# Performance work log

Measured on AMD Instinct MI355X. Metric: run time of the kernel, lower is better.

## Reference

```python
import jax, jax.numpy as jnp
import numpy as np

CHANNELS = 10
LENGTH = 64
DEPTH = 4
BATCH = 2048


def setup_inputs() -> dict:
    key = jax.random.key(0)
    x = jax.random.normal(key, (BATCH, CHANNELS * LENGTH), dtype=jnp.float32)
    return {"x": x}


def _seg_exp(dx, depth):
    # Signature of a single linear segment with increment dx: (B, C).
    # Level k is dx^{(x)k} / k! (flattened to (B, C^k)).
    b = dx.shape[0]
    terms = [dx]
    for k in range(2, depth + 1):
        t = jnp.einsum('bi,bj->bij', terms[-1], dx).reshape(b, -1) / k
        terms.append(t)
    return tuple(terms)


def _chen(a, b, depth):
    # Truncated tensor-algebra product (Chen's identity), both with scalar part 1.
    # (A (x) B)_k = A_k + B_k + sum_{i=1}^{k-1} A_i (x) B_{k-i}
    bsz = a[0].shape[0]
    out = []
    for k in range(1, depth + 1):
        t = a[k - 1] + b[k - 1]
        for i in range(1, k):
            t = t + jnp.einsum('bi,bj->bij', a[i - 1], b[k - i - 1]).reshape(bsz, -1)
        out.append(t)
    return tuple(out)


def signature(path, depth):
    # path: (B, C, L). Increments along the path (last) dimension.
    dx = (path[:, :, 1:] - path[:, :, :-1]).transpose(0, 2, 1)  # (B, L-1, C)
    init = _seg_exp(dx[:, 0], depth)

    def step(carry, dxt):
        return _chen(carry, _seg_exp(dxt, depth), depth), None

    sig, _ = jax.lax.scan(step, init, dx[:, 1:].transpose(1, 0, 2))  # scan over L-2 steps
    return jnp.concatenate(sig, axis=-1)  # (B, sum_k C^k)


def reference(x):
    path = x.reshape(x.shape[0], CHANNELS, LENGTH)
    return signature(path, DEPTH)
```

## Files before the change

### kernel.cpp

```cpp
#include <hip/hip_runtime.h>
#include <hip/hip_bf16.h>


typedef short short8 __attribute__((ext_vector_type(8)));
typedef float f2 __attribute__((ext_vector_type(2)));
typedef float f4 __attribute__((ext_vector_type(4)));
typedef float f32x4 __attribute__((ext_vector_type(4)));
typedef unsigned int uint4v __attribute__((ext_vector_type(4)));

constexpr int C = 10, L = 64, T = 63;
constexpr int OUTSZ = 10 + 100 + 1000 + 10000;
constexpr int SP = 68;
constexpr int KS = 64;

__device__ __forceinline__ unsigned packbf(float lo, float hi) {
  union { __hip_bfloat162 h; unsigned u; } cv;
  cv.h = __float22bfloat162_rn(make_float2(lo, hi));
  return cv.u;
}
__device__ __forceinline__ int swz(int row, int k) {
  return row * KS + ((((k >> 3) ^ (row & 7)) << 3) | (k & 7));
}

__global__ __launch_bounds__(512, 6) void sig4_kernel(
    const float* __restrict__ x, float* __restrict__ out)
{
  __shared__ __align__(16) unsigned char smem_raw[45120];
  unsigned short* Ab = (unsigned short*)smem_raw;
  unsigned short* Ub = (unsigned short*)(smem_raw + 12800);
  unsigned short* Bb = (unsigned short*)(smem_raw + 25600);
  float* dxT = (float*)(smem_raw + 39680);
  float* PsT = (float*)(smem_raw + 42400);

  const int t = threadIdx.x;
  const int w = t >> 6, lane = t & 63;
  const float* __restrict__ xb = x + (size_t)blockIdx.x * (C * L);
  float* __restrict__ ob = out + (size_t)blockIdx.x * OUTSZ;

  for (int i = t; i < C * SP; i += 512) {
    int c = i / SP, s = i - c * SP;
    float v = 0.f;
    if (s < T) v = xb[c * L + s + 1] - xb[c * L + s];
    dxT[i] = v;
  }
  __syncthreads();
  for (int c = w; c < C; c += 8) {
    float v = (lane > 0) ? dxT[c * SP + lane - 1] : 0.f;
    #pragma unroll
    for (int d = 1; d < 64; d <<= 1) {
      float y = __shfl_up(v, d);
      if (lane >= d) v += y;
    }
    PsT[c * SP + lane] = v;
  }
  if (t < 40) PsT[(t >> 2) * SP + 64 + (t & 3)] = 0.f;
  __syncthreads();

  if (t < 100) {
    const int i_ = t / 10, j_ = t - (t / 10) * 10;
    const float* dip = dxT + i_ * SP;
    const float* pp  = PsT + i_ * SP;
    const float* djp = dxT + j_ * SP;
    float s2 = 0.f;
    #pragma unroll
    for (int ch = 0; ch < 8; ++ch) {
      f4 d0 = *(const f4*)(dip + ch * 8), d1 = *(const f4*)(dip + ch * 8 + 4);
      f4 p0 = *(const f4*)(pp  + ch * 8), p1 = *(const f4*)(pp  + ch * 8 + 4);
      f4 e0 = *(const f4*)(djp + ch * 8), e1 = *(const f4*)(djp + ch * 8 + 4);
      float di[8] = {d0.x, d0.y, d0.z, d0.w, d1.x, d1.y, d1.z, d1.w};
      float pv[8] = {p0.x, p0.y, p0.z, p0.w, p1.x, p1.y, p1.z, p1.w};
      float dj[8] = {e0.x, e0.y, e0.z, e0.w, e1.x, e1.y, e1.z, e1.w};
      float bu[8], bv[8], zz[8];
      #pragma unroll
      for (int e = 0; e < 8; ++e) {
        bu[e] = fmaf(di[e], 0.25f, pv[e]) * (dj[e] * (1.f / 3.f));
        bv[e] = fmaf(di[e], (1.f / 3.f), pv[e]) * (dj[e] * 0.5f);
        zz[e] = fmaf(di[e], 0.5f, pv[e]) * dj[e];
      }
      float u2v[8], v2v[8];
      #pragma unroll
      for (int e = 0; e < 8; ++e) {
        u2v[e] = bu[e] + s2;
        v2v[e] = bv[e] + s2;
        s2 += zz[e];
      }
      uint4v vp, up;
      #pragma unroll
      for (int q = 0; q < 4; ++q) {
        vp[q] = packbf(v2v[2 * q], v2v[2 * q + 1]);
        up[q] = packbf(u2v[2 * q], u2v[2 * q + 1]);
      }
      *(uint4v*)&Ab[swz(t, ch * 8)] = vp;
      *(uint4v*)&Ub[swz(t, ch * 8)] = up;
    }
    ob[10 + t] = s2;
    if (j_ == 0) ob[i_] = PsT[i_ * SP + 63];
  } else if (t >= 128) {
    const int q = t - 128;
    for (int task = q; task < 110 * 8; task += 384) {
      const int col = task >> 3, ch = task & 7;
      const int base = ch * 8;
      float b1v[8];
      if (col < 100) {
        const int k2 = col / 10, l2 = col - (col / 10) * 10;
        const float* dk = dxT + k2 * SP;
        const float* pl = PsT + l2 * SP;
        const float S1l = pl[63];
        f4 d0 = *(const f4*)(dk + base), d1 = *(const f4*)(dk + base + 4);
        f4 pa = *(const f4*)(pl + base), pb = *(const f4*)(pl + base + 4);
        f4 pc = *(const f4*)(pl + base + 8);
        float dv[8] = {d0.x, d0.y, d0.z, d0.w, d1.x, d1.y, d1.z, d1.w};
        float Pn[8] = {pa.y, pa.z, pa.w, pb.x, pb.y, pb.z, pb.w, pc.x};
        #pragma unroll
        for (int e = 0; e < 8; ++e) b1v[e] = dv[e] * (S1l - Pn[e]);
      } else {
        const float* dk = dxT + (col - 100) * SP;
        f4 d0 = *(const f4*)(dk + base), d1 = *(const f4*)(dk + base + 4);
        b1v[0] = d0.x; b1v[1] = d0.y; b1v[2] = d0.z; b1v[3] = d0.w;
        b1v[4] = d1.x; b1v[5] = d1.y; b1v[6] = d1.z; b1v[7] = d1.w;
      }
      uint4v pk;
      #pragma unroll
      for (int qq = 0; qq < 4; ++qq) pk[qq] = packbf(b1v[2 * qq], b1v[2 * qq + 1]);
      *(uint4v*)&Bb[swz(col, base)] = pk;
    }
  }
  __syncthreads();

  const int lm = lane & 15, lg = lane >> 4;
  f32x4 acc[7];
  #pragma unroll
  for (int ct = 0; ct < 7; ++ct) acc[ct] = f32x4{0.f, 0.f, 0.f, 0.f};

  if (w < 7) {
    const int arow = w * 16 + lm;
    short8 a0 = (arow < 100) ? *(const short8*)&Ab[swz(arow, lg * 8)]
                             : short8{0, 0, 0, 0, 0, 0, 0, 0};
    short8 a1 = (arow < 100) ? *(const short8*)&Ab[swz(arow, 32 + lg * 8)]
                             : short8{0, 0, 0, 0, 0, 0, 0, 0};
    #pragma unroll
    for (int ct = 0; ct < 7; ++ct) {
      const int bcol = ct * 16 + lm;
      short8 b0 = (bcol < 110) ? *(const short8*)&Bb[swz(bcol, lg * 8)]
                               : short8{0, 0, 0, 0, 0, 0, 0, 0};
      short8 b1 = (bcol < 110) ? *(const short8*)&Bb[swz(bcol, 32 + lg * 8)]
                               : short8{0, 0, 0, 0, 0, 0, 0, 0};
      acc[ct] = __builtin_amdgcn_mfma_f32_16x16x32_bf16(b0, a0, acc[ct], 0, 0, 0);
      acc[ct] = __builtin_amdgcn_mfma_f32_16x16x32_bf16(b1, a1, acc[ct], 0, 0, 0);
    }
  }
  __syncthreads();

  for (int task = t; task < 110 * 8; task += 512) {
    const int col = task >> 3, ch = task & 7;
    const int base = ch * 8;
    float b2v[8] = {0.f, 0.f, 0.f, 0.f, 0.f, 0.f, 0.f, 0.f};
    if (col < 100) {
      const int k2 = col / 10, l2 = col - (col / 10) * 10;
      const float* dk = dxT + k2 * SP;
      const float* dl = dxT + l2 * SP;
      f4 a0 = *(const f4*)(dk + base), a1 = *(const f4*)(dk + base + 4);
      f4 c0 = *(const f4*)(dl + base), c1 = *(const f4*)(dl + base + 4);
      b2v[0] = a0.x * c0.x * 0.5f; b2v[1] = a0.y * c0.y * 0.5f;
      b2v[2] = a0.z * c0.z * 0.5f; b2v[3] = a0.w * c0.w * 0.5f;
      b2v[4] = a1.x * c1.x * 0.5f; b2v[5] = a1.y * c1.y * 0.5f;
      b2v[6] = a1.z * c1.z * 0.5f; b2v[7] = a1.w * c1.w * 0.5f;
    }
    uint4v pk;
    #pragma unroll
    for (int qq = 0; qq < 4; ++qq) pk[qq] = packbf(b2v[2 * qq], b2v[2 * qq + 1]);
    *(uint4v*)&Bb[swz(col, base)] = pk;
  }
  __syncthreads();

  if (w < 7) {
    const int arow = w * 16 + lm;
    short8 a0 = (arow < 100) ? *(const short8*)&Ub[swz(arow, lg * 8)]
                             : short8{0, 0, 0, 0, 0, 0, 0, 0};
    short8 a1 = (arow < 100) ? *(const short8*)&Ub[swz(arow, 32 + lg * 8)]
                             : short8{0, 0, 0, 0, 0, 0, 0, 0};
    #pragma unroll
    for (int ct = 0; ct < 7; ++ct) {
      const int bcol = ct * 16 + lm;
      short8 b0 = (bcol < 110) ? *(const short8*)&Bb[swz(bcol, lg * 8)]
                               : short8{0, 0, 0, 0, 0, 0, 0, 0};
      short8 b1 = (bcol < 110) ? *(const short8*)&Bb[swz(bcol, 32 + lg * 8)]
                               : short8{0, 0, 0, 0, 0, 0, 0, 0};
      acc[ct] = __builtin_amdgcn_mfma_f32_16x16x32_bf16(b0, a0, acc[ct], 0, 0, 0);
      acc[ct] = __builtin_amdgcn_mfma_f32_16x16x32_bf16(b1, a1, acc[ct], 0, 0, 0);
    }

    const int row = w * 16 + lm;
    if (row < 100) {
      float* rowp4 = ob + 1110 + row * 100;
      float* rowp3 = ob + 110 + row * 10;
      #pragma unroll
      for (int ct = 0; ct < 7; ++ct) {
        const int colbase = ct * 16 + lg * 4;
        f2 lo = {acc[ct][0], acc[ct][1]};
        f2 hi = {acc[ct][2], acc[ct][3]};
        if (colbase < 100) {
          *(f2*)(rowp4 + colbase) = lo;
          *(f2*)(rowp4 + colbase + 2) = hi;
        } else if (colbase < 110) {
          *(f2*)(rowp3 + (colbase - 100)) = lo;
          if (colbase < 108) *(f2*)(rowp3 + (colbase - 98)) = hi;
        }
      }
    }
  }
}

extern "C" void kernel_launch(void* const* d_in, const int* in_sizes, int n_in,
                              void* d_out, int out_size, void* d_ws, size_t ws_size,
                              hipStream_t stream) {
  const float* x = (const float*)d_in[0];
  float* out = (float*)d_out;
  const int batch = in_sizes[0] / (C * L);
  sig4_kernel<<<dim3(batch), dim3(512), 0, stream>>>(x, out);
}
```

Baseline: 33.83 us.

## Merge two K=64 MFMA passes into one K=128 GEMM with concatenated operands

Concatenates the A/U operands and the two B operand sets along K into 128-wide swizzled LDS tiles, so both matrix products run in a single MFMA pass. Both B halves are built in one producer loop. This removes two block-wide barriers, the separate B2 rebuild phase and the extra accumulator round. In exchange LDS use grows from about 45 KB to 59 KB and the launch-bounds occupancy hint drops from 6 to 4, which may reduce resident blocks per CU.

```diff
diff --git a/kernel.cpp b/kernel.cpp
--- a/kernel.cpp
+++ b/kernel.cpp
@@ -11,7 +11,7 @@
 constexpr int C = 10, L = 64, T = 63;
 constexpr int OUTSZ = 10 + 100 + 1000 + 10000;
 constexpr int SP = 68;
-constexpr int KS = 64;
+constexpr int KS = 128;
 
 __device__ __forceinline__ unsigned packbf(float lo, float hi) {
   union { __hip_bfloat162 h; unsigned u; } cv;
@@ -22,15 +22,14 @@
   return row * KS + ((((k >> 3) ^ (row & 7)) << 3) | (k & 7));
 }
 
-__global__ __launch_bounds__(512, 6) void sig4_kernel(
+__global__ __launch_bounds__(512, 4) void sig4_kernel(
     const float* __restrict__ x, float* __restrict__ out)
 {
-  __shared__ __align__(16) unsigned char smem_raw[45120];
+  __shared__ __align__(16) unsigned char smem_raw[59200];
   unsigned short* Ab = (unsigned short*)smem_raw;
-  unsigned short* Ub = (unsigned short*)(smem_raw + 12800);
   unsigned short* Bb = (unsigned short*)(smem_raw + 25600);
-  float* dxT = (float*)(smem_raw + 39680);
-  float* PsT = (float*)(smem_raw + 42400);
+  float* dxT = (float*)(smem_raw + 53760);
+  float* PsT = (float*)(smem_raw + 56480);
 
   const int t = threadIdx.x;
   const int w = t >> 6, lane = t & 63;
@@ -90,104 +89,80 @@
         vp[q] = packbf(v2v[2 * q], v2v[2 * q + 1]);
         up[q] = packbf(u2v[2 * q], u2v[2 * q + 1]);
       }
-      *(uint4v*)&Ab[swz(t, ch * 8)] = vp;
-      *(uint4v*)&Ub[swz(t, ch * 8)] = up;
+      *(uint4v*)&Ab[swz(t, ch * 8)]      = vp;
+      *(uint4v*)&Ab[swz(t, 64 + ch * 8)] = up;
     }
     ob[10 + t] = s2;
     if (j_ == 0) ob[i_] = PsT[i_ * SP + 63];
   } else if (t >= 128) {
     const int q = t - 128;
-    for (int task = q; task < 110 * 8; task += 384) {
-      const int col = task >> 3, ch = task & 7;
-      const int base = ch * 8;
-      float b1v[8];
-      if (col < 100) {
-        const int k2 = col / 10, l2 = col - (col / 10) * 10;
-        const float* dk = dxT + k2 * SP;
-        const float* pl = PsT + l2 * SP;
-        const float S1l = pl[63];
-        f4 d0 = *(const f4*)(dk + base), d1 = *(const f4*)(dk + base + 4);
-        f4 pa = *(const f4*)(pl + base), pb = *(const f4*)(pl + base + 4);
-        f4 pc = *(const f4*)(pl + base + 8);
-        float dv[8] = {d0.x, d0.y, d0.z, d0.w, d1.x, d1.y, d1.z, d1.w};
-        float Pn[8] = {pa.y, pa.z, pa.w, pb.x, pb.y, pb.z, pb.w, pc.x};
-        #pragma unroll
-        for (int e = 0; e < 8; ++e) b1v[e] = dv[e] * (S1l - Pn[e]);
+    for (int task = q; task < 110 * 16; task += 384) {
+      const int col = task >> 4, ch = task & 15;
+      const int base = (ch & 7) * 8;
+      float bval[8];
+      if (ch < 8) {
+        if (col < 100) {
+          const int k2 = col / 10, l2 = col - (col / 10) * 10;
+          const float* dk = dxT + k2 * SP;
+          const float* pl = PsT + l2 * SP;
+          const float S1l = pl[63];
+          f4 d0 = *(const f4*)(dk + base), d1 = *(const f4*)(dk + base + 4);
+          f4 pa = *(const f4*)(pl + base + 1), pb = *(const f4*)(pl + base + 5);
+          float dv[8] = {d0.x, d0.y, d0.z, d0.w, d1.x, d1.y, d1.z, d1.w};
+          float Pn[8] = {pa.x, pa.y, pa.z, pa.w, pb.x, pb.y, pb.z, pb.w};
+          #pragma unroll
+          for (int e = 0; e < 8; ++e) bval[e] = dv[e] * (S1l - Pn[e]);
+        } else {
+          const float* dk = dxT + (col - 100) * SP;
+          f4 d0 = *(const f4*)(dk + base), d1 = *(const f4*)(dk + base + 4);
+          bval[0] = d0.x; bval[1] = d0.y; bval[2] = d0.z; bval[3] = d0.w;
+          bval[4] = d1.x; bval[5] = d1.y; bval[6] = d1.z; bval[7] = d1.w;
+        }
       } else {
-        const float* dk = dxT + (col - 100) * SP;
-        f4 d0 = *(const f4*)(dk + base), d1 = *(const f4*)(dk + base + 4);
-        b1v[0] = d0.x; b1v[1] = d0.y; b1v[2] = d0.z; b1v[3] = d0.w;
-        b1v[4] = d1.x; b1v[5] = d1.y; b1v[6] = d1.z; b1v[7] = d1.w;
+        if (col < 100) {
+          const int k2 = col / 10, l2 = col - (col / 10) * 10;
+          const float* dk = dxT + k2 * SP;
+          const float* dl = dxT + l2 * SP;
+          f4 a0 = *(const f4*)(dk + base), a1 = *(const f4*)(dk + base + 4);
+          f4 c0 = *(const f4*)(dl + base), c1 = *(const f4*)(dl + base + 4);
+          bval[0] = a0.x * c0.x * 0.5f; bval[1] = a0.y * c0.y * 0.5f;
+          bval[2] = a0.z * c0.z * 0.5f; bval[3] = a0.w * c0.w * 0.5f;
+          bval[4] = a1.x * c1.x * 0.5f; bval[5] = a1.y * c1.y * 0.5f;
+          bval[6] = a1.z * c1.z * 0.5f; bval[7] = a1.w * c1.w * 0.5f;
+        } else {
+          #pragma unroll
+          for (int e = 0; e < 8; ++e) bval[e] = 0.f;
+        }
       }
+      const int kbase = (ch < 8) ? base : (64 + base);
       uint4v pk;
       #pragma unroll
-      for (int qq = 0; qq < 4; ++qq) pk[qq] = packbf(b1v[2 * qq], b1v[2 * qq + 1]);
-      *(uint4v*)&Bb[swz(col, base)] = pk;
+      for (int qq = 0; qq < 4; ++qq) pk[qq] = packbf(bval[2 * qq], bval[2 * qq + 1]);
+      *(uint4v*)&Bb[swz(col, kbase)] = pk;
     }
   }
   __syncthreads();
 
-  const int lm = lane & 15, lg = lane >> 4;
-  f32x4 acc[7];
-  #pragma unroll
-  for (int ct = 0; ct < 7; ++ct) acc[ct] = f32x4{0.f, 0.f, 0.f, 0.f};
-
   if (w < 7) {
+    const int lm = lane & 15, lg = lane >> 4;
     const int arow = w * 16 + lm;
-    short8 a0 = (arow < 100) ? *(const short8*)&Ab[swz(arow, lg * 8)]
-                             : short8{0, 0, 0, 0, 0, 0, 0, 0};
-    short8 a1 = (arow < 100) ? *(const short8*)&Ab[swz(arow, 32 + lg * 8)]
-                             : short8{0, 0, 0, 0, 0, 0, 0, 0};
+    short8 a[4];
+    #pragma unroll
+    for (int ks = 0; ks < 4; ++ks)
+      a[ks] = (arow < 100) ? *(const short8*)&Ab[swz(arow, ks * 32 + lg * 8)]
+                           : short8{0, 0, 0, 0, 0, 0, 0, 0};
+    f32x4 acc[7];
     #pragma unroll
     for (int ct = 0; ct < 7; ++ct) {
       const int bcol = ct * 16 + lm;
-      short8 b0 = (bcol < 110) ? *(const short8*)&Bb[swz(bcol, lg * 8)]
-                               : short8{0, 0, 0, 0, 0, 0, 0, 0};
-      short8 b1 = (bcol < 110) ? *(const short8*)&Bb[swz(bcol, 32 + lg * 8)]
-                               : short8{0, 0, 0, 0, 0, 0, 0, 0};
-      acc[ct] = __builtin_amdgcn_mfma_f32_16x16x32_bf16(b0, a0, acc[ct], 0, 0, 0);
-      acc[ct] = __builtin_amdgcn_mfma_f32_16x16x32_bf16(b1, a1, acc[ct], 0, 0, 0);
-    }
-  }
-  __syncthreads();
-
-  for (int task = t; task < 110 * 8; task += 512) {
-    const int col = task >> 3, ch = task & 7;
-    const int base = ch * 8;
-    float b2v[8] = {0.f, 0.f, 0.f, 0.f, 0.f, 0.f, 0.f, 0.f};
-    if (col < 100) {
-      const int k2 = col / 10, l2 = col - (col / 10) * 10;
-      const float* dk = dxT + k2 * SP;
-      const float* dl = dxT + l2 * SP;
-      f4 a0 = *(const f4*)(dk + base), a1 = *(const f4*)(dk + base + 4);
-      f4 c0 = *(const f4*)(dl + base), c1 = *(const f4*)(dl + base + 4);
-      b2v[0] = a0.x * c0.x * 0.5f; b2v[1] = a0.y * c0.y * 0.5f;
-      b2v[2] = a0.z * c0.z * 0.5f; b2v[3] = a0.w * c0.w * 0.5f;
-      b2v[4] = a1.x * c1.x * 0.5f; b2v[5] = a1.y * c1.y * 0.5f;
-      b2v[6] = a1.z * c1.z * 0.5f; b2v[7] = a1.w * c1.w * 0.5f;
-    }
-    uint4v pk;
-    #pragma unroll
-    for (int qq = 0; qq < 4; ++qq) pk[qq] = packbf(b2v[2 * qq], b2v[2 * qq + 1]);
-    *(uint4v*)&Bb[swz(col, base)] = pk;
-  }
-  __syncthreads();
-
-  if (w < 7) {
-    const int arow = w * 16 + lm;
-    short8 a0 = (arow < 100) ? *(const short8*)&Ub[swz(arow, lg * 8)]
-                             : short8{0, 0, 0, 0, 0, 0, 0, 0};
-    short8 a1 = (arow < 100) ? *(const short8*)&Ub[swz(arow, 32 + lg * 8)]
-                             : short8{0, 0, 0, 0, 0, 0, 0, 0};
-    #pragma unroll
-    for (int ct = 0; ct < 7; ++ct) {
-      const int bcol = ct * 16 + lm;
-      short8 b0 = (bcol < 110) ? *(const short8*)&Bb[swz(bcol, lg * 8)]
-                               : short8{0, 0, 0, 0, 0, 0, 0, 0};
-      short8 b1 = (bcol < 110) ? *(const short8*)&Bb[swz(bcol, 32 + lg * 8)]
-                               : short8{0, 0, 0, 0, 0, 0, 0, 0};
-      acc[ct] = __builtin_amdgcn_mfma_f32_16x16x32_bf16(b0, a0, acc[ct], 0, 0, 0);
-      acc[ct] = __builtin_amdgcn_mfma_f32_16x16x32_bf16(b1, a1, acc[ct], 0, 0, 0);
+      acc[ct] = f32x4{0.f, 0.f, 0.f, 0.f};
+      #pragma unroll
+      for (int ks = 0; ks < 4; ++ks) {
+        short8 bf = (bcol < 110)
+            ? *(const short8*)&Bb[swz(bcol, ks * 32 + lg * 8)]
+            : short8{0, 0, 0, 0, 0, 0, 0, 0};
+        acc[ct] = __builtin_amdgcn_mfma_f32_16x16x32_bf16(bf, a[ks], acc[ct], 0, 0, 0);
+      }
     }
 
     const int row = w * 16 + lm;
```

Result: slower. 39.80 us (+17.7%).
